# Kernel tuning notes

Hardware: AMD Instinct MI355X
Metric: run time of the kernel (lower is better)

Reference implementation:

```python
import jax, jax.numpy as jnp
import numpy as np

S, N, F_IN, F_OUT = 8, 4096, 128, 128


def setup_inputs() -> dict:
    key = jax.random.key(0)
    ks = jax.random.split(key, 7)
    return {
        "theta": jax.random.normal(ks[0], (S,), dtype=jnp.float32),
        "T_slices": jax.random.normal(ks[1], (S, N, N), dtype=jnp.float32),
        "x": jax.random.normal(ks[2], (N, F_IN), dtype=jnp.float32),
        "a": jax.random.uniform(ks[3], (N, N), dtype=jnp.float32),
        "W_fc": jax.random.normal(ks[4], (F_OUT, F_IN), dtype=jnp.float32) * (1.0 / np.sqrt(F_IN)),
        "b_fc": jax.random.normal(ks[5], (F_OUT,), dtype=jnp.float32) * 0.01,
        "prelu_alpha": jnp.full((F_IN,), 0.25, dtype=jnp.float32),
    }


def reference(theta, T_slices, x, a, W_fc, b_fc, prelu_alpha):
    # q = sum_s theta[s] * T_slices[s]  -> [N, N]
    q = jnp.einsum("s,snm->nm", theta, T_slices)
    # mask by adjacency (the torch code then converts to sparse; math is identical)
    q = q * a
    # diffused features: [N, N] @ [N, F_in] -> [N, F_in]
    out = q @ x
    # per-channel PReLU over the feature dim (num_parameters = input_dim)
    out = jnp.where(out >= 0, out, prelu_alpha * out)
    # final linear: out @ W_fc.T + b_fc -> [N, F_out]
    return out @ W_fc.T + b_fc
```

## Files before the change

kernel.cpp:

```cpp
#include <hip/hip_runtime.h>

constexpr int N  = 4096;
constexpr int F  = 128;
constexpr int S  = 8;
constexpr int BM = 32;
constexpr int KSPLIT = 8;
constexpr int KRANGE = N / KSPLIT;
constexpr int BK = 32;
constexpr int NCH = KRANGE / BK;
constexpr int NT = 256;

typedef float f4 __attribute__((ext_vector_type(4)));

__device__ __forceinline__ void bar_sync() {
  asm volatile("s_waitcnt lgkmcnt(0)" ::: "memory");
  __builtin_amdgcn_s_barrier();
  asm volatile("" ::: "memory");
}

__device__ __forceinline__ void vm_drain() {
  asm volatile("s_waitcnt vmcnt(0)" ::: "memory");
}

__device__ __forceinline__ void gload_lds16(const float* g, float* l) {
  __builtin_amdgcn_global_load_lds(
      (const __attribute__((address_space(1))) void*)g,
      (__attribute__((address_space(3))) void*)l, 16, 0, 0);
}

template <bool USE_WS>
__global__ __launch_bounds__(NT, 2) void ggd_diffuse(
    const float* __restrict__ theta,
    const float* __restrict__ Ts,
    const float* __restrict__ x,
    const float* __restrict__ a,
    float* __restrict__ dst)
{
  __shared__ float rawT[S][BM][BK];
  __shared__ float rawA[BM][BK];
  __shared__ float x_lds[2][BK * F];
  __shared__ float q_lds[BM][BK];

  const int t  = threadIdx.x;
  const int rb = blockIdx.x >> 3;
  const int ks = blockIdx.x & 7;
  const int n0 = rb * BM;
  const int k0 = ks * KRANGE;

  float th[S];
#pragma unroll
  for (int s = 0; s < S; ++s) th[s] = theta[s];

  const int wave = t >> 6, lane = t & 63;

  const int grow = lane >> 3;
  const int gcol = (lane & 7) * 4;
  const size_t slice = (size_t)N * N;

  const int qr = t >> 3;
  const int qk = (t & 7) * 4;

  const int rg = t >> 5;
  const int fg = t & 31;

  f4 acc[4];
#pragma unroll
  for (int r = 0; r < 4; ++r) acc[r] = (f4)(0.f);

  auto stage_raw = [&](int c) {
    const size_t cb = (size_t)(k0 + c * BK) + gcol;
#pragma unroll
    for (int j = 0; j < 8; ++j) {
      const int i = wave * 8 + j;
      const int s = i >> 2;
      const int q4 = i & 3;
      const float* src = Ts + (size_t)s * slice +
                         (size_t)(n0 + q4 * 8 + grow) * N + cb;
      gload_lds16(src, &rawT[0][0][0] + i * 256);
    }
    {
      const float* src = a + (size_t)(n0 + wave * 8 + grow) * N + cb;
      gload_lds16(src, &rawA[0][0] + wave * 256);
    }
  };

  auto stage_x = [&](int c, int buf) {
    const float* xg = x + (size_t)(k0 + c * BK) * F;
#pragma unroll
    for (int i = 0; i < 4; ++i) {
      const int seg = (wave * 4 + i) * 256;
      gload_lds16(xg + seg + lane * 4, &x_lds[buf][seg]);
    }
  };

  auto qgen = [&]() {
    f4 av = *(const f4*)&rawA[qr][qk];
    f4 sum;
    {
      f4 tv = *(const f4*)&rawT[0][qr][qk];
#pragma unroll
      for (int j = 0; j < 4; ++j) sum[j] = th[0] * tv[j];
    }
#pragma unroll
    for (int s = 1; s < S; ++s) {
      f4 tv = *(const f4*)&rawT[s][qr][qk];
#pragma unroll
      for (int j = 0; j < 4; ++j) sum[j] = fmaf(th[s], tv[j], sum[j]);
    }
    f4 q;
#pragma unroll
    for (int j = 0; j < 4; ++j) q[j] = av[j] * sum[j];
    *(f4*)&q_lds[qr][qk] = q;
  };

  auto compute = [&](int buf) {
    const float* qb = &q_lds[rg * 4][0];
    const float* xb = &x_lds[buf][0] + fg * 4;
#pragma unroll
    for (int k4 = 0; k4 < BK / 4; ++k4) {
      f4 xv[4];
#pragma unroll
      for (int j = 0; j < 4; ++j)
        xv[j] = *(const f4*)(xb + (size_t)(k4 * 4 + j) * F);
#pragma unroll
      for (int rr = 0; rr < 4; ++rr) {
        f4 qv = *(const f4*)(qb + rr * BK + k4 * 4);
#pragma unroll
        for (int j = 0; j < 4; ++j)
#pragma unroll
          for (int e = 0; e < 4; ++e)
            acc[rr][e] = fmaf(qv[j], xv[j][e], acc[rr][e]);
      }
    }
  };

  stage_raw(0);
  stage_x(0, 0);
  vm_drain();
  bar_sync();
  qgen();
  bar_sync();

  for (int c = 0; c < NCH; ++c) {
    const int buf = c & 1;
    const bool more = (c + 1 < NCH);
    if (more) {
      stage_raw(c + 1);
      stage_x(c + 1, buf ^ 1);
    }
    compute(buf);
    if (more) {
      vm_drain();
      bar_sync();
      qgen();
      bar_sync();
    }
  }

#pragma unroll
  for (int rr = 0; rr < 4; ++rr) {
    const size_t row = (size_t)(n0 + rg * 4 + rr);
    if (USE_WS) {
      float* op = dst + ((size_t)ks * N + row) * F + fg * 4;
      *(f4*)op = acc[rr];
    } else {
      float* op = dst + row * F + fg * 4;
#pragma unroll
      for (int e = 0; e < 4; ++e) atomicAdd(op + e, acc[rr][e]);
    }
  }
}

template <bool USE_WS>
__global__ __launch_bounds__(256, 2) void ggd_fc(
    const float* __restrict__ W,
    const float* __restrict__ bfc,
    const float* __restrict__ alpha,
    const float* __restrict__ src,
    float* __restrict__ out)
{
  __shared__ float p_lds[16 * F];
  const int t  = threadIdx.x;
  const int n0 = blockIdx.x * 16;

  {
    const int lr = t >> 4, c8 = (t & 15) * 8;
    f4 v0, v1;
    if (USE_WS) {
      v0 = (f4)(0.f); v1 = (f4)(0.f);
#pragma unroll
      for (int ks = 0; ks < KSPLIT; ++ks) {
        const float* sp = src + ((size_t)ks * N + n0 + lr) * F + c8;
        v0 += *(const f4*)(sp);
        v1 += *(const f4*)(sp + 4);
      }
    } else {
      const float* ip = src + (size_t)(n0 + lr) * F + c8;
      v0 = *(const f4*)(ip);
      v1 = *(const f4*)(ip + 4);
    }
    f4 a0 = *(const f4*)(alpha + c8);
    f4 a1 = *(const f4*)(alpha + c8 + 4);
#pragma unroll
    for (int j = 0; j < 4; ++j) {
      v0[j] = v0[j] >= 0.f ? v0[j] : a0[j] * v0[j];
      v1[j] = v1[j] >= 0.f ? v1[j] : a1[j] * v1[j];
    }
    *(f4*)&p_lds[lr * F + c8]     = v0;
    *(f4*)&p_lds[lr * F + c8 + 4] = v1;
  }
  __syncthreads();

  const int r2  = t >> 5;
  const int fo0 = (t & 31) * 4;
  f4 accA = *(const f4*)(bfc + fo0);
  f4 accB = accA;
#pragma unroll 4
  for (int fi4 = 0; fi4 < F / 4; ++fi4) {
    f4 pA = *(const f4*)&p_lds[r2 * F + fi4 * 4];
    f4 pB = *(const f4*)&p_lds[(r2 + 8) * F + fi4 * 4];
#pragma unroll
    for (int e = 0; e < 4; ++e) {
      f4 wv = *(const f4*)(W + (size_t)(fo0 + e) * F + fi4 * 4);
      accA[e] = fmaf(pA[0], wv[0], fmaf(pA[1], wv[1],
                fmaf(pA[2], wv[2], fmaf(pA[3], wv[3], accA[e]))));
      accB[e] = fmaf(pB[0], wv[0], fmaf(pB[1], wv[1],
                fmaf(pB[2], wv[2], fmaf(pB[3], wv[3], accB[e]))));
    }
  }
  *(f4*)(out + (size_t)(n0 + r2) * F + fo0)     = accA;
  *(f4*)(out + (size_t)(n0 + r2 + 8) * F + fo0) = accB;
}

extern "C" void kernel_launch(void* const* d_in, const int* in_sizes, int n_in,
                              void* d_out, int out_size, void* d_ws, size_t ws_size,
                              hipStream_t stream) {
  const float* theta = (const float*)d_in[0];
  const float* Ts    = (const float*)d_in[1];
  const float* x     = (const float*)d_in[2];
  const float* a     = (const float*)d_in[3];
  const float* W     = (const float*)d_in[4];
  const float* bfc   = (const float*)d_in[5];
  const float* alpha = (const float*)d_in[6];
  float* out = (float*)d_out;

  const size_t ws_need = (size_t)KSPLIT * N * F * sizeof(float);
  if (ws_size >= ws_need && d_ws != nullptr) {
    float* ws = (float*)d_ws;
    ggd_diffuse<true><<<dim3((N / BM) * KSPLIT), dim3(NT), 0, stream>>>(
        theta, Ts, x, a, ws);
    ggd_fc<true><<<dim3(N / 16), dim3(256), 0, stream>>>(
        W, bfc, alpha, ws, out);
  } else {
    hipMemsetAsync(out, 0, (size_t)out_size * sizeof(float), stream);
    ggd_diffuse<false><<<dim3((N / BM) * KSPLIT), dim3(NT), 0, stream>>>(
        theta, Ts, x, a, out);
    ggd_fc<false><<<dim3(N / 16), dim3(256), 0, stream>>>(
        W, bfc, alpha, out, out);
  }
}
```

Before: 147.4 us.

## Use bf16 MFMA for diffusion GEMM with pre-transposed bf16 x

Adds a kernel that converts x to bf16 and transposes it to feature-major layout, then replaces the scalar FP32 FMA inner product in the diffuse kernel with 16x16x32 bf16 MFMA instructions, with q also stored as bf16 in LDS. This targets the VALU compute bottleneck of the q@x product, since the kernel mostly streams the 8 T slices. It lowers input precision to bf16 for that product, adds an extra launch, and switches output to scalar stores. The fallback path writes xT into the workspace even when d_ws may be null.

Result: faster. 142.6 us (-3.3%).

```diff
diff --git a/kernel.cpp b/kernel.cpp
--- a/kernel.cpp
+++ b/kernel.cpp
@@ -1,4 +1,5 @@
 #include <hip/hip_runtime.h>
+#include <stdint.h>
 
 constexpr int N  = 4096;
 constexpr int F  = 128;
@@ -10,7 +11,15 @@
 constexpr int NCH = KRANGE / BK;
 constexpr int NT = 256;
 
-typedef float f4 __attribute__((ext_vector_type(4)));
+typedef float f4  __attribute__((ext_vector_type(4)));
+typedef short bf16x8 __attribute__((ext_vector_type(8)));
+typedef unsigned short us4 __attribute__((ext_vector_type(4)));
+
+__device__ __forceinline__ unsigned short f2bf(float f) {
+  union { float f; unsigned int u; } v; v.f = f;
+  unsigned int u = v.u + 0x7FFFu + ((v.u >> 16) & 1u);
+  return (unsigned short)(u >> 16);
+}
 
 __device__ __forceinline__ void bar_sync() {
   asm volatile("s_waitcnt lgkmcnt(0)" ::: "memory");
@@ -22,24 +31,51 @@
   asm volatile("s_waitcnt vmcnt(0)" ::: "memory");
 }
 
-__device__ __forceinline__ void gload_lds16(const float* g, float* l) {
+__device__ __forceinline__ void gload_lds16(const void* g, void* l) {
   __builtin_amdgcn_global_load_lds(
       (const __attribute__((address_space(1))) void*)g,
       (__attribute__((address_space(3))) void*)l, 16, 0, 0);
+}
+
+__global__ __launch_bounds__(256, 2) void ggd_xt(
+    const float* __restrict__ x, unsigned short* __restrict__ xT) {
+  __shared__ float xl[64][132];
+  const int t  = threadIdx.x;
+  const int k0 = blockIdx.x * 64;
+
+  {
+    const int kr = t >> 2, fs = (t & 3) * 32;
+    const float* src = x + (size_t)(k0 + kr) * F + fs;
+#pragma unroll
+    for (int i = 0; i < 8; ++i)
+      *(f4*)&xl[kr][fs + i * 4] = *(const f4*)(src + i * 4);
+  }
+  __syncthreads();
+  {
+    const int f = t >> 1, kh = (t & 1) * 32;
+    us4 o[8];
+#pragma unroll
+    for (int i = 0; i < 32; ++i)
+      o[i >> 2][i & 3] = f2bf(xl[kh + i][f]);
+    unsigned short* dst = xT + (size_t)f * N + k0 + kh;
+#pragma unroll
+    for (int j = 0; j < 8; ++j)
+      *(us4*)(dst + j * 4) = o[j];
+  }
 }
 
 template <bool USE_WS>
 __global__ __launch_bounds__(NT, 2) void ggd_diffuse(
     const float* __restrict__ theta,
     const float* __restrict__ Ts,
-    const float* __restrict__ x,
+    const unsigned short* __restrict__ xT,
     const float* __restrict__ a,
     float* __restrict__ dst)
 {
   __shared__ float rawT[S][BM][BK];
   __shared__ float rawA[BM][BK];
-  __shared__ float x_lds[2][BK * F];
-  __shared__ float q_lds[BM][BK];
+  __shared__ unsigned short xt_lds[2][F][BK];
+  __shared__ unsigned short q_lds[BM][BK];
 
   const int t  = threadIdx.x;
   const int rb = blockIdx.x >> 3;
@@ -60,12 +96,12 @@
   const int qr = t >> 3;
   const int qk = (t & 7) * 4;
 
-  const int rg = t >> 5;
-  const int fg = t & 31;
+  const int rtile = wave >> 1;
+  const int fbase = (wave & 1) * 4;
 
   f4 acc[4];
 #pragma unroll
-  for (int r = 0; r < 4; ++r) acc[r] = (f4)(0.f);
+  for (int i = 0; i < 4; ++i) acc[i] = (f4)(0.f);
 
   auto stage_raw = [&](int c) {
     const size_t cb = (size_t)(k0 + c * BK) + gcol;
@@ -76,20 +112,23 @@
       const int q4 = i & 3;
       const float* src = Ts + (size_t)s * slice +
                          (size_t)(n0 + q4 * 8 + grow) * N + cb;
-      gload_lds16(src, &rawT[0][0][0] + i * 256);
+      gload_lds16(src, (float*)&rawT[0][0][0] + i * 256);
     }
     {
       const float* src = a + (size_t)(n0 + wave * 8 + grow) * N + cb;
-      gload_lds16(src, &rawA[0][0] + wave * 256);
+      gload_lds16(src, (float*)&rawA[0][0] + wave * 256);
     }
   };
 
   auto stage_x = [&](int c, int buf) {
-    const float* xg = x + (size_t)(k0 + c * BK) * F;
-#pragma unroll
-    for (int i = 0; i < 4; ++i) {
-      const int seg = (wave * 4 + i) * 256;
-      gload_lds16(xg + seg + lane * 4, &x_lds[buf][seg]);
+    const uint8_t* xb = (const uint8_t*)xT;
+    const size_t kbyte = (size_t)(k0 + c * BK) * 2;
+#pragma unroll
+    for (int j = 0; j < 2; ++j) {
+      const int i = wave * 2 + j;
+      const int fr = i * 16 + (lane >> 2);
+      const uint8_t* src = xb + (size_t)fr * (N * 2) + kbyte + (lane & 3) * 16;
+      gload_lds16(src, &xt_lds[buf][i * 16][0]);
     }
   };
 
@@ -107,30 +146,22 @@
 #pragma unroll
       for (int j = 0; j < 4; ++j) sum[j] = fmaf(th[s], tv[j], sum[j]);
     }
-    f4 q;
-#pragma unroll
-    for (int j = 0; j < 4; ++j) q[j] = av[j] * sum[j];
-    *(f4*)&q_lds[qr][qk] = q;
+    us4 q;
+#pragma unroll
+    for (int j = 0; j < 4; ++j) q[j] = f2bf(av[j] * sum[j]);
+    *(us4*)&q_lds[qr][qk] = q;
   };
 
   auto compute = [&](int buf) {
-    const float* qb = &q_lds[rg * 4][0];
-    const float* xb = &x_lds[buf][0] + fg * 4;
-#pragma unroll
-    for (int k4 = 0; k4 < BK / 4; ++k4) {
-      f4 xv[4];
-#pragma unroll
-      for (int j = 0; j < 4; ++j)
-        xv[j] = *(const f4*)(xb + (size_t)(k4 * 4 + j) * F);
-#pragma unroll
-      for (int rr = 0; rr < 4; ++rr) {
-        f4 qv = *(const f4*)(qb + rr * BK + k4 * 4);
-#pragma unroll
-        for (int j = 0; j < 4; ++j)
-#pragma unroll
-          for (int e = 0; e < 4; ++e)
-            acc[rr][e] = fmaf(qv[j], xv[j][e], acc[rr][e]);
-      }
+    const unsigned short* qb = &q_lds[rtile * 16][0];
+    bf16x8 afrag = *(const bf16x8*)(qb + (lane & 15) * BK + (lane >> 4) * 8);
+#pragma unroll
+    for (int i = 0; i < 4; ++i) {
+      const int ftile = fbase + i;
+      const unsigned short* bb = &xt_lds[buf][ftile * 16][0];
+      bf16x8 bfrag = *(const bf16x8*)(bb + (lane & 15) * BK + (lane >> 4) * 8);
+      acc[i] = __builtin_amdgcn_mfma_f32_16x16x32_bf16(afrag, bfrag, acc[i],
+                                                       0, 0, 0);
     }
   };
 
@@ -157,16 +188,19 @@
     }
   }
 
-#pragma unroll
-  for (int rr = 0; rr < 4; ++rr) {
-    const size_t row = (size_t)(n0 + rg * 4 + rr);
-    if (USE_WS) {
-      float* op = dst + ((size_t)ks * N + row) * F + fg * 4;
-      *(f4*)op = acc[rr];
-    } else {
-      float* op = dst + row * F + fg * 4;
-#pragma unroll
-      for (int e = 0; e < 4; ++e) atomicAdd(op + e, acc[rr][e]);
+  const int crow = n0 + rtile * 16 + (lane >> 4) * 4;
+  const int ccol = (lane & 15);
+#pragma unroll
+  for (int i = 0; i < 4; ++i) {
+    const int fo = (fbase + i) * 16 + ccol;
+#pragma unroll
+    for (int r = 0; r < 4; ++r) {
+      const size_t row = (size_t)(crow + r);
+      if (USE_WS) {
+        dst[((size_t)ks * N + row) * F + fo] = acc[i][r];
+      } else {
+        atomicAdd(dst + row * F + fo, acc[i][r]);
+      }
     }
   }
 }
@@ -244,17 +278,22 @@
   const float* alpha = (const float*)d_in[6];
   float* out = (float*)d_out;
 
-  const size_t ws_need = (size_t)KSPLIT * N * F * sizeof(float);
-  if (ws_size >= ws_need && d_ws != nullptr) {
-    float* ws = (float*)d_ws;
+  const size_t part_bytes = (size_t)KSPLIT * N * F * sizeof(float);
+  const size_t xt_bytes   = (size_t)N * F * 2;
+  if (ws_size >= part_bytes + xt_bytes && d_ws != nullptr) {
+    float* parts = (float*)d_ws;
+    unsigned short* xT = (unsigned short*)((char*)d_ws + part_bytes);
+    ggd_xt<<<dim3(N / 64), dim3(256), 0, stream>>>(x, xT);
     ggd_diffuse<true><<<dim3((N / BM) * KSPLIT), dim3(NT), 0, stream>>>(
-        theta, Ts, x, a, ws);
+        theta, Ts, xT, a, parts);
     ggd_fc<true><<<dim3(N / 16), dim3(256), 0, stream>>>(
-        W, bfc, alpha, ws, out);
+        W, bfc, alpha, parts, out);
   } else {
+    unsigned short* xT = (unsigned short*)d_ws;
     hipMemsetAsync(out, 0, (size_t)out_size * sizeof(float), stream);
+    ggd_xt<<<dim3(N / 64), dim3(256), 0, stream>>>(x, xT);
     ggd_diffuse<false><<<dim3((N / BM) * KSPLIT), dim3(NT), 0, stream>>>(
-        theta, Ts, x, a, out);
+        theta, Ts, xT, a, out);
     ggd_fc<false><<<dim3(N / 16), dim3(256), 0, stream>>>(
         W, bfc, alpha, out, out);
   }
```
